# Kernel optimization log

Hardware: AMD Instinct MI355X
Metric: run time of the kernel (lower is better)

Reference implementation:

```python
import jax, jax.numpy as jnp
import numpy as np

B, L, D, H = 4, 1024, 1024, 16
DH = D // H  # 64
TOPK = 32


def setup_inputs() -> dict:
    key = jax.random.key(0)
    ks = jax.random.split(key, 9)
    s = 1.0 / np.sqrt(D)
    return {
        "x": jax.random.normal(ks[0], (B, L, D), jnp.float32),
        "Wq": jax.random.normal(ks[1], (D, D), jnp.float32) * s,
        "bq": jax.random.normal(ks[2], (D,), jnp.float32) * 0.01,
        "Wk": jax.random.normal(ks[3], (D, D), jnp.float32) * s,
        "bk": jax.random.normal(ks[4], (D,), jnp.float32) * 0.01,
        "Wv": jax.random.normal(ks[5], (D, D), jnp.float32) * s,
        "bv": jax.random.normal(ks[6], (D,), jnp.float32) * 0.01,
        "Wo": jax.random.normal(ks[7], (D, D), jnp.float32) * s,
        "bo": jax.random.normal(ks[8], (D,), jnp.float32) * 0.01,
        "top_k": TOPK,
    }


def reference(x, Wq, bq, Wk, bk, Wv, bv, Wo, bo, top_k):
    b, l, _ = x.shape
    q = (x @ Wq + bq).reshape(b, l, H, DH)
    k = (x @ Wk + bk).reshape(b, l, H, DH)
    v = (x @ Wv + bv).reshape(b, l, H, DH)
    # scores: [B, i, j, h]
    scores = jnp.einsum('bihd,bjhd->bijh', q, k) / np.sqrt(DH).astype(np.float32)
    # softmax over axis 2 (j), as in the original (dim=2 of bijh)
    weights = jax.nn.softmax(scores, axis=2)
    if top_k is not None:
        # top-k along j: move j to last axis -> [B, i, h, j]
        w_t = jnp.swapaxes(weights, 2, 3)
        _, idx = jax.lax.top_k(w_t, top_k)
        mask = jnp.put_along_axis(jnp.zeros_like(w_t), idx, 1.0, axis=-1, inplace=False)
        w_t = w_t * mask
        w_t = w_t / (jnp.sum(w_t, axis=-1, keepdims=True) + 1e-8)
        weights = jnp.swapaxes(w_t, 2, 3)
    attn = jnp.einsum('bijh,bjhd->bihd', weights, v).reshape(b, l, D)
    return attn @ Wo + bo
```

## Files before the change

### kernel.cpp

```cpp
#include <hip/hip_runtime.h>
#include <math.h>

#define B_ 4
#define L_ 1024
#define D_ 1024
#define H_ 16
#define DH_ 64
#define M_ (B_*L_)

typedef _Float16 half8 __attribute__((ext_vector_type(8)));
typedef _Float16 half4 __attribute__((ext_vector_type(4)));
typedef float f32x4 __attribute__((ext_vector_type(4)));

#define MFMA16(a,b,c) __builtin_amdgcn_mfma_f32_16x16x32_f16(a, b, c, 0, 0, 0)

__device__ __forceinline__ void glds16(const void* g, const void* s) {
  __builtin_amdgcn_global_load_lds(
      (const __attribute__((address_space(1))) uint32_t*)g,
      (__attribute__((address_space(3))) uint32_t*)(uintptr_t)s,
      16, 0, 0);
}

#define DPPF(oldv, x, ctrl, rmask) \
  __int_as_float(__builtin_amdgcn_update_dpp(__float_as_int(oldv), __float_as_int(x), ctrl, rmask, 0xf, false))

__device__ __forceinline__ float wfred_max(float x) {
  x = fmaxf(x, DPPF(-INFINITY, x, 0x111, 0xf));
  x = fmaxf(x, DPPF(-INFINITY, x, 0x112, 0xf));
  x = fmaxf(x, DPPF(-INFINITY, x, 0x114, 0xf));
  x = fmaxf(x, DPPF(-INFINITY, x, 0x118, 0xf));
  x = fmaxf(x, DPPF(-INFINITY, x, 0x142, 0xa));
  x = fmaxf(x, DPPF(-INFINITY, x, 0x143, 0xc));
  return __int_as_float(__builtin_amdgcn_readlane(__float_as_int(x), 63));
}
__device__ __forceinline__ float wfred_sum(float x) {
  x = x + DPPF(0.f, x, 0x111, 0xf);
  x = x + DPPF(0.f, x, 0x112, 0xf);
  x = x + DPPF(0.f, x, 0x114, 0xf);
  x = x + DPPF(0.f, x, 0x118, 0xf);
  x = x + DPPF(0.f, x, 0x142, 0xa);
  x = x + DPPF(0.f, x, 0x143, 0xc);
  return __int_as_float(__builtin_amdgcn_readlane(__float_as_int(x), 63));
}

__global__ __launch_bounds__(256) void split_x(const float* __restrict__ x,
                                               _Float16* __restrict__ xh,
                                               _Float16* __restrict__ xl) {
  const int i = blockIdx.x * 256 + threadIdx.x;
  float4 v = ((const float4*)x)[i];
  const float a0 = v.x * 16.f, a1 = v.y * 16.f, a2 = v.z * 16.f, a3 = v.w * 16.f;
  const _Float16 h0 = (_Float16)a0, h1 = (_Float16)a1, h2 = (_Float16)a2, h3 = (_Float16)a3;
  half4 hv, lv;
  hv[0] = h0; hv[1] = h1; hv[2] = h2; hv[3] = h3;
  lv[0] = (_Float16)(a0 - (float)h0);
  lv[1] = (_Float16)(a1 - (float)h1);
  lv[2] = (_Float16)(a2 - (float)h2);
  lv[3] = (_Float16)(a3 - (float)h3);
  ((half4*)xh)[i] = hv;
  ((half4*)xl)[i] = lv;
}

__global__ __launch_bounds__(256) void split_w4(const float* __restrict__ W0,
                                                const float* __restrict__ W1,
                                                const float* __restrict__ W2,
                                                const float* __restrict__ W3,
                                                _Float16* __restrict__ Whl_base) {
  const int z = blockIdx.z;
  const float* W = (z == 0) ? W0 : (z == 1) ? W1 : (z == 2) ? W2 : W3;
  _Float16* Wh = Whl_base + (size_t)z * 2 * (size_t)(D_ * D_);
  _Float16* Wl = Wh + (size_t)(D_ * D_);
  __shared__ float tile[64][65];
  const int t = threadIdx.x;
  const int tk = blockIdx.x & 15;
  const int tn = blockIdx.x >> 4;
  const int kr = t >> 2, ns = (t & 3) * 16;
  const float* src = W + (size_t)(tk * 64 + kr) * D_ + tn * 64 + ns;
  float4 v0 = ((const float4*)src)[0];
  float4 v1 = ((const float4*)src)[1];
  float4 v2 = ((const float4*)src)[2];
  float4 v3 = ((const float4*)src)[3];
  tile[ns + 0][kr] = v0.x;  tile[ns + 1][kr] = v0.y;  tile[ns + 2][kr] = v0.z;  tile[ns + 3][kr] = v0.w;
  tile[ns + 4][kr] = v1.x;  tile[ns + 5][kr] = v1.y;  tile[ns + 6][kr] = v1.z;  tile[ns + 7][kr] = v1.w;
  tile[ns + 8][kr] = v2.x;  tile[ns + 9][kr] = v2.y;  tile[ns + 10][kr] = v2.z; tile[ns + 11][kr] = v2.w;
  tile[ns + 12][kr] = v3.x; tile[ns + 13][kr] = v3.y; tile[ns + 14][kr] = v3.z; tile[ns + 15][kr] = v3.w;
  __syncthreads();
  const int nr = t >> 2, ks = (t & 3) * 16;
  const float* tr = &tile[nr][ks];
  half8 hv0, hv1, lv0, lv1;
#pragma unroll
  for (int i = 0; i < 8; i++) {
    const float s0 = tr[i] * 512.f;
    const float s1 = tr[i + 8] * 512.f;
    const _Float16 h0 = (_Float16)s0, h1 = (_Float16)s1;
    hv0[i] = h0; hv1[i] = h1;
    lv0[i] = (_Float16)(s0 - (float)h0);
    lv1[i] = (_Float16)(s1 - (float)h1);
  }
  _Float16* dh = Wh + (size_t)(tn * 64 + nr) * D_ + tk * 64 + ks;
  _Float16* dl = Wl + (size_t)(tn * 64 + nr) * D_ + tk * 64 + ks;
  *(half8*)dh = hv0; *(half8*)(dh + 8) = hv1;
  *(half8*)dl = lv0; *(half8*)(dl + 8) = lv1;
}

__device__ __forceinline__ void gemm_f16x3_body(
    const _Float16* __restrict__ Ah, const _Float16* __restrict__ Al,
    const _Float16* __restrict__ Bh, const _Float16* __restrict__ Bl,
    const float* __restrict__ bias, float* __restrict__ Cf,
    _Float16* __restrict__ Ch, _Float16* __restrict__ Cl, const bool f16out) {
  __shared__ __align__(16) _Float16 sA[2][2][128][32];
  __shared__ __align__(16) _Float16 sB[2][2][128][32];
  const int t = threadIdx.x;
  const int lane = t & 63;
  const int wid = t >> 6;
  const int bm = blockIdx.y * 128;
  const int bn = blockIdx.x * 128;

  const int m0 = t >> 2, sp0 = t & 3;
  const int sl0 = sp0 ^ ((m0 >> 1) & 3);
  const int m1 = m0 + 64;
  const _Float16* gA0h = Ah + (size_t)(bm + m0) * D_ + sl0 * 8;
  const _Float16* gA1h = Ah + (size_t)(bm + m1) * D_ + sl0 * 8;
  const _Float16* gA0l = Al + (size_t)(bm + m0) * D_ + sl0 * 8;
  const _Float16* gA1l = Al + (size_t)(bm + m1) * D_ + sl0 * 8;
  const _Float16* gB0h = Bh + (size_t)(bn + m0) * D_ + sl0 * 8;
  const _Float16* gB1h = Bh + (size_t)(bn + m1) * D_ + sl0 * 8;
  const _Float16* gB0l = Bl + (size_t)(bn + m0) * D_ + sl0 * 8;
  const _Float16* gB1l = Bl + (size_t)(bn + m1) * D_ + sl0 * 8;

  char* sAb = (char*)&sA[0][0][0][0];
  char* sBb = (char*)&sB[0][0][0][0];
  const int wvb = (t >> 6) * 1024;

#define STAGE(pp, kk) do { \
    glds16(gA0h + (kk), sAb + (pp) * 16384 + wvb); \
    glds16(gA1h + (kk), sAb + (pp) * 16384 + 4096 + wvb); \
    glds16(gA0l + (kk), sAb + (pp) * 16384 + 8192 + wvb); \
    glds16(gA1l + (kk), sAb + (pp) * 16384 + 12288 + wvb); \
    glds16(gB0h + (kk), sBb + (pp) * 16384 + wvb); \
    glds16(gB1h + (kk), sBb + (pp) * 16384 + 4096 + wvb); \
    glds16(gB0l + (kk), sBb + (pp) * 16384 + 8192 + wvb); \
    glds16(gB1l + (kk), sBb + (pp) * 16384 + 12288 + wvb); \
  } while (0)

  STAGE(0, 0);
  __syncthreads();

  f32x4 acc[4][4];
#pragma unroll
  for (int i = 0; i < 4; i++)
#pragma unroll
    for (int j = 0; j < 4; j++) acc[i][j] = {0.f, 0.f, 0.f, 0.f};

  const int wr = wid >> 1, wc = wid & 1;
  const int l15 = lane & 15;
  const int soff = ((lane >> 4) ^ ((l15 >> 1) & 3)) * 8;

  int p = 0;
  for (int k0 = 0; k0 < 1024; k0 += 32) {
    const bool more = (k0 + 32) < 1024;
    if (more) STAGE(p ^ 1, k0 + 32);
    half8 bh[4], bl[4];
#pragma unroll
    for (int ni = 0; ni < 4; ni++) {
      const int rb = wc * 64 + ni * 16 + l15;
      bh[ni] = *(const half8*)&sB[p][0][rb][soff];
      bl[ni] = *(const half8*)&sB[p][1][rb][soff];
    }
#pragma unroll
    for (int mi = 0; mi < 4; mi++) {
      const int ra = wr * 64 + mi * 16 + l15;
      const half8 ah = *(const half8*)&sA[p][0][ra][soff];
      const half8 al = *(const half8*)&sA[p][1][ra][soff];
#pragma unroll
      for (int ni = 0; ni < 4; ni++) {
        acc[mi][ni] = MFMA16(ah, bh[ni], acc[mi][ni]);
        acc[mi][ni] = MFMA16(ah, bl[ni], acc[mi][ni]);
        acc[mi][ni] = MFMA16(al, bh[ni], acc[mi][ni]);
      }
    }
    if (more) {
      __syncthreads();
      p ^= 1;
    }
  }
#undef STAGE

  const float inv = 1.0f / 8192.0f;
  const int orow = bm + wr * 64 + (lane >> 4) * 4;
  const int ocol = bn + wc * 64 + l15;
#pragma unroll
  for (int ni = 0; ni < 4; ni++) {
    const int col = ocol + ni * 16;
    const float bv = bias[col];
#pragma unroll
    for (int mi = 0; mi < 4; mi++) {
      const f32x4 a = acc[mi][ni];
#pragma unroll
      for (int r = 0; r < 4; r++) {
        const size_t idx = (size_t)(orow + mi * 16 + r) * D_ + col;
        const float val = a[r] * inv + bv;
        if (f16out) {
          const float vs = val * 16.0f;
          const _Float16 hh = (_Float16)vs;
          Ch[idx] = hh;
          Cl[idx] = (_Float16)(vs - (float)hh);
        } else {
          Cf[idx] = val;
        }
      }
    }
  }
}

__global__ __launch_bounds__(256, 2) void gemm_qkv_f16(
    const _Float16* __restrict__ xh, const _Float16* __restrict__ xl,
    const _Float16* __restrict__ Whq, const _Float16* __restrict__ Wlq,
    const _Float16* __restrict__ Whk, const _Float16* __restrict__ Wlk,
    const _Float16* __restrict__ Whv, const _Float16* __restrict__ Wlv,
    const float* __restrict__ bq, const float* __restrict__ bk, const float* __restrict__ bv,
    _Float16* __restrict__ qh, _Float16* __restrict__ ql,
    _Float16* __restrict__ kh, _Float16* __restrict__ kl,
    float* __restrict__ vf) {
  const int z = blockIdx.z;
  const _Float16* Bh = (z == 0) ? Whq : (z == 1) ? Whk : Whv;
  const _Float16* Bl = (z == 0) ? Wlq : (z == 1) ? Wlk : Wlv;
  const float* bias = (z == 0) ? bq : (z == 1) ? bk : bv;
  if (z == 2) {
    gemm_f16x3_body(xh, xl, Bh, Bl, bias, vf, nullptr, nullptr, false);
  } else {
    _Float16* Ch = (z == 0) ? qh : kh;
    _Float16* Cl = (z == 0) ? ql : kl;
    gemm_f16x3_body(xh, xl, Bh, Bl, bias, nullptr, Ch, Cl, true);
  }
}

__global__ __launch_bounds__(256, 2) void gemm_out_f16(
    const _Float16* __restrict__ ah, const _Float16* __restrict__ al,
    const _Float16* __restrict__ bh, const _Float16* __restrict__ bl,
    const float* __restrict__ bias, float* __restrict__ C) {
  gemm_f16x3_body(ah, al, bh, bl, bias, C, nullptr, nullptr, false);
}

#define SSWZ(row) (((row) & 7) << 2)

__global__ __launch_bounds__(512, 4) void attn_topk_mfma(
    const _Float16* __restrict__ qh, const _Float16* __restrict__ ql,
    const _Float16* __restrict__ kh, const _Float16* __restrict__ kl,
    const float* __restrict__ vf,
    _Float16* __restrict__ awh, _Float16* __restrict__ awl) {
  __shared__ float S[8][1024];
  __shared__ int   cidx[8][64];
  __shared__ float cfe[8][64];
  const int t = threadIdx.x;
  const int lane = t & 63;
  const int w = t >> 6;
  const int id = blockIdx.x;
  const int wk = (id & 7) * 1024 + (id >> 3);
  const int it = wk & 127;
  const int bh = wk >> 7;
  const int h = bh & 15;
  const int b = bh >> 4;
  const int i0 = it * 8;
  const size_t rowbase = (size_t)b * L_;
  const int l15 = lane & 15;
  const int kgrp = lane >> 4;

  half8 Ahf[2], Alf[2];
#pragma unroll
  for (int ks = 0; ks < 2; ks++) {
    const size_t off = (rowbase + i0 + (l15 & 7)) * D_ + h * DH_ + ks * 32 + kgrp * 8;
    Ahf[ks] = *(const half8*)(qh + off);
    Alf[ks] = *(const half8*)(ql + off);
  }

  const float sscale = 1.0f / 2048.0f;
  for (int jt = 0; jt < 8; jt++) {
    const int j0 = w * 128 + jt * 16;
    const size_t koff = (rowbase + j0 + l15) * D_ + h * DH_ + kgrp * 8;
    const half8 Bh0 = *(const half8*)(kh + koff);
    const half8 Bh1 = *(const half8*)(kh + koff + 32);
    const half8 Bl0 = *(const half8*)(kl + koff);
    const half8 Bl1 = *(const half8*)(kl + koff + 32);
    f32x4 acc = {0.f, 0.f, 0.f, 0.f};
    acc = MFMA16(Ahf[0], Bh0, acc);
    acc = MFMA16(Ahf[1], Bh1, acc);
    acc = MFMA16(Ahf[0], Bl0, acc);
    acc = MFMA16(Ahf[1], Bl1, acc);
    acc = MFMA16(Alf[0], Bh0, acc);
    acc = MFMA16(Alf[1], Bh1, acc);
    if (kgrp < 2) {
      const int srow = kgrp * 4;
#pragma unroll
      for (int r = 0; r < 4; r++)
        S[srow + r][(j0 + l15) ^ SSWZ(srow + r)] = acc[r] * sscale;
    }
  }
  __syncthreads();

  const int row = w;
  const int swz = SSWZ(row);
  float sc[16];
#pragma unroll
  for (int u = 0; u < 16; u++) sc[u] = S[row][(u * 64 + lane) ^ swz];

  float mx;
  {
    float m = sc[0];
#pragma unroll
    for (int u = 1; u < 16; u++) m = fmaxf(m, sc[u]);
    mx = wfred_max(m);
  }

  float lo = mx - 16.f, hi = mx;
  for (int it2 = 0; it2 < 12; ++it2) {
    float mid = 0.5f * (lo + hi);
    int cnt = 0;
#pragma unroll
    for (int u = 0; u < 16; u++) cnt += __popcll(__ballot(sc[u] >= mid));
    if (cnt >= 32) lo = mid; else hi = mid;
  }
  int cabove = 0;
#pragma unroll
  for (int u = 0; u < 16; u++) cabove += __popcll(__ballot(sc[u] >= hi));
  float v31 = hi;
  while (cabove < 32) {
    float nx = -INFINITY;
#pragma unroll
    for (int u = 0; u < 16; u++) nx = fmaxf(nx, (sc[u] < v31) ? sc[u] : -INFINITY);
    nx = wfred_max(nx);
    int ceq = 0;
#pragma unroll
    for (int u = 0; u < 16; u++) ceq += __popcll(__ballot(sc[u] == nx));
    cabove += ceq;
    v31 = nx;
  }
  int c_eq = 0;
#pragma unroll
  for (int u = 0; u < 16; u++) c_eq += __popcll(__ballot(sc[u] == v31));
  const int c_gt = cabove - c_eq;
  const bool span = (cabove > 32);
  const int keep_eq = 32 - c_gt;
  float v32;
  if (span) {
    v32 = v31;
  } else {
    float nx = -INFINITY;
#pragma unroll
    for (int u = 0; u < 16; u++) nx = fmaxf(nx, (sc[u] < v31) ? sc[u] : -INFINITY);
    nx = wfred_max(nx);
    v32 = nx;
  }
  const float tau = 0.5f * (v31 + v32);
  const float invbeta = 166666.67f;

  float e_[16];
#pragma unroll
  for (int u = 0; u < 16; u++) e_[u] = __expf(sc[u] - mx);
  float z = 0.f;
#pragma unroll
  for (int u = 0; u < 16; u++) z += e_[u];
  z = wfred_sum(z);

  bool band = false;
  if (!span) {
    int inband = 0;
#pragma unroll
    for (int u = 0; u < 16; u++)
      inband |= (fabsf(sc[u] - tau) <= 1.81e-4f) ? 1 : 0;
    band = (__ballot(inband) != 0ull);
  }

  const float cutoff = fminf(tau - 1.8e-4f, v31);
  const float* vcol = vf + rowbase * D_ + h * DH_ + lane;
  float o;
  bool fast = false;
  if (!span) {
    int run = 0;
    float psum = 0.f;
#pragma unroll
    for (int u = 0; u < 16; u++) {
      unsigned long long m = __ballot(sc[u] >= cutoff);
      if (sc[u] >= cutoff) {
        float feu;
        if (band) {
          float arg = (sc[u] - tau) * invbeta;
          float fwv = (arg > 30.f) ? 1.f : ((arg < -30.f) ? 0.f : 1.f / (1.f + __expf(-arg)));
          feu = fwv * e_[u];
        } else {
          feu = (sc[u] > tau) ? e_[u] : 0.f;
        }
        int pos = run + (int)__popcll(m & ((1ull << lane) - 1ull));
        if (pos < 64) { cidx[row][pos] = u * 64 + lane; cfe[row][pos] = feu; }
        psum += feu;
      }
      run += (int)__popcll(m);
    }
    if (run <= 64) {
      fast = true;
      const int npad = (run + 7) & ~7;
      if (lane < npad - run) { cidx[row][run + lane] = 0; cfe[row][run + lane] = 0.f; }
      const int nch = npad >> 3;
      auto ldc = [&](int c, int* J, float* F) {
#pragma unroll
        for (int i = 0; i < 8; i++) { J[i] = cidx[row][c * 8 + i]; F[i] = cfe[row][c * 8 + i]; }
      };
      auto ldv = [&](const int* J, float* V) {
#pragma unroll
        for (int i = 0; i < 8; i++) V[i] = vcol[(size_t)J[i] * D_];
      };
      auto fm8 = [&](const float* F, const float* V, float& a) {
#pragma unroll
        for (int i = 0; i < 8; i++) a = fmaf(F[i], V[i], a);
      };
      int jA[8], jB[8]; float fA[8], fB[8], vA[8], vB[8];
      float accv = 0.f;
      ldc(0, jA, fA); ldv(jA, vA);
      for (int c = 0; c < nch; c += 2) {
        if (c + 1 < nch) { ldc(c + 1, jB, fB); ldv(jB, vB); }
        fm8(fA, vA, accv);
        if (c + 2 < nch) { ldc(c + 2, jA, fA); ldv(jA, vA); }
        if (c + 1 < nch) fm8(fB, vB, accv);
      }
      const float Ssum = wfred_sum(psum);
      o = accv / (Ssum + 1e-8f * z);
    }
  }
  if (!fast) {
    float Ssum = 0.f, acc = 0.f;
    int eq_seen = 0;
    for (int u = 0; u < 16; ++u) {
      unsigned long long mask = __ballot(sc[u] >= cutoff);
      while (mask) {
        int l2 = (int)__builtin_ctzll(mask);
        mask &= mask - 1;
        float s_ = __shfl(sc[u], l2, 64);
        float e2 = __expf(s_ - mx);
        float f_;
        if (span) {
          if (s_ > v31) f_ = 1.f;
          else if (s_ == v31) { f_ = (eq_seen < keep_eq) ? 1.f : 0.f; ++eq_seen; }
          else f_ = 0.f;
        } else {
          float arg = (s_ - tau) * invbeta;
          f_ = (arg > 30.f) ? 1.f : ((arg < -30.f) ? 0.f : 1.f / (1.f + __expf(-arg)));
        }
        float fe_ = f_ * e2;
        Ssum += fe_;
        acc = fmaf(fe_, vcol[(size_t)(u * 64 + l2) * D_], acc);
      }
    }
    o = acc / (Ssum + 1e-8f * z);
  }

  const float os = o * 16.0f;
  const _Float16 oh = (_Float16)os;
  const size_t oidx = (rowbase + i0 + row) * D_ + h * DH_ + lane;
  awh[oidx] = oh;
  awl[oidx] = (_Float16)(os - (float)oh);
}

extern "C" void kernel_launch(void* const* d_in, const int* in_sizes, int n_in,
                              void* d_out, int out_size, void* d_ws, size_t ws_size,
                              hipStream_t stream) {
  const float* x  = (const float*)d_in[0];
  const float* Wq = (const float*)d_in[1];
  const float* bq = (const float*)d_in[2];
  const float* Wk = (const float*)d_in[3];
  const float* bk = (const float*)d_in[4];
  const float* Wv = (const float*)d_in[5];
  const float* bv = (const float*)d_in[6];
  const float* Wo = (const float*)d_in[7];
  const float* bo = (const float*)d_in[8];
  float* out = (float*)d_out;

  const size_t MD = (size_t)M_ * D_;
  const size_t WD = (size_t)D_ * D_;
  float* slot0 = (float*)d_ws;
  float* slot1 = slot0 + MD;
  float* vf    = slot1 + MD;
  float* slot3 = vf + MD;
  float* slot4 = slot3 + MD;

  _Float16* qh = (_Float16*)slot0;  _Float16* ql = qh + MD;
  _Float16* kh = (_Float16*)slot1;  _Float16* kl = kh + MD;
  _Float16* xh = (_Float16*)slot3;  _Float16* xl = xh + MD;
  _Float16* awh = xh;
  _Float16* awl = xl;
  _Float16* Wsplit = (_Float16*)slot4;
  _Float16* Whq = Wsplit;
  _Float16* Wlq = Whq + WD;
  _Float16* Whk = Wlq + WD;
  _Float16* Wlk = Whk + WD;
  _Float16* Whv = Wlk + WD;
  _Float16* Wlv = Whv + WD;
  _Float16* Who = Wlv + WD;
  _Float16* Wlo = Who + WD;

  dim3 b256(256);
  hipLaunchKernelGGL(split_x, dim3(4096), b256, 0, stream, x, xh, xl);
  hipLaunchKernelGGL(split_w4, dim3(256, 1, 4), b256, 0, stream, Wq, Wk, Wv, Wo, Wsplit);
  hipLaunchKernelGGL(gemm_qkv_f16, dim3(8, 32, 3), b256, 0, stream,
                     xh, xl, Whq, Wlq, Whk, Wlk, Whv, Wlv, bq, bk, bv,
                     qh, ql, kh, kl, vf);
  hipLaunchKernelGGL(attn_topk_mfma, dim3(8192), dim3(512), 0, stream,
                     qh, ql, kh, kl, vf, awh, awl);
  hipLaunchKernelGGL(gemm_out_f16, dim3(8, 32), b256, 0, stream,
                     awh, awl, Who, Wlo, bo, out);
}
```

Baseline: 504.9 us.

## Single-buffer GEMM LDS for higher occupancy, pack attention candidates, add MFMA priority

Result: slower. 529.6 us (+4.9%).

```diff
diff --git a/kernel.cpp b/kernel.cpp
--- a/kernel.cpp
+++ b/kernel.cpp
@@ -107,8 +107,8 @@
     const _Float16* __restrict__ Bh, const _Float16* __restrict__ Bl,
     const float* __restrict__ bias, float* __restrict__ Cf,
     _Float16* __restrict__ Ch, _Float16* __restrict__ Cl, const bool f16out) {
-  __shared__ __align__(16) _Float16 sA[2][2][128][32];
-  __shared__ __align__(16) _Float16 sB[2][2][128][32];
+  __shared__ __align__(16) _Float16 sA[2][128][32];
+  __shared__ __align__(16) _Float16 sB[2][128][32];
   const int t = threadIdx.x;
   const int lane = t & 63;
   const int wid = t >> 6;
@@ -127,23 +127,20 @@
   const _Float16* gB0l = Bl + (size_t)(bn + m0) * D_ + sl0 * 8;
   const _Float16* gB1l = Bl + (size_t)(bn + m1) * D_ + sl0 * 8;
 
-  char* sAb = (char*)&sA[0][0][0][0];
-  char* sBb = (char*)&sB[0][0][0][0];
-  const int wvb = (t >> 6) * 1024;
-
-#define STAGE(pp, kk) do { \
-    glds16(gA0h + (kk), sAb + (pp) * 16384 + wvb); \
-    glds16(gA1h + (kk), sAb + (pp) * 16384 + 4096 + wvb); \
-    glds16(gA0l + (kk), sAb + (pp) * 16384 + 8192 + wvb); \
-    glds16(gA1l + (kk), sAb + (pp) * 16384 + 12288 + wvb); \
-    glds16(gB0h + (kk), sBb + (pp) * 16384 + wvb); \
-    glds16(gB1h + (kk), sBb + (pp) * 16384 + 4096 + wvb); \
-    glds16(gB0l + (kk), sBb + (pp) * 16384 + 8192 + wvb); \
-    glds16(gB1l + (kk), sBb + (pp) * 16384 + 12288 + wvb); \
+  char* sAb = (char*)&sA[0][0][0];
+  char* sBb = (char*)&sB[0][0][0];
+  const int wvb = wid * 1024;
+
+#define STAGE(kk) do { \
+    glds16(gA0h + (kk), sAb + wvb); \
+    glds16(gA1h + (kk), sAb + 4096 + wvb); \
+    glds16(gA0l + (kk), sAb + 8192 + wvb); \
+    glds16(gA1l + (kk), sAb + 12288 + wvb); \
+    glds16(gB0h + (kk), sBb + wvb); \
+    glds16(gB1h + (kk), sBb + 4096 + wvb); \
+    glds16(gB0l + (kk), sBb + 8192 + wvb); \
+    glds16(gB1l + (kk), sBb + 12288 + wvb); \
   } while (0)
-
-  STAGE(0, 0);
-  __syncthreads();
 
   f32x4 acc[4][4];
 #pragma unroll
@@ -155,32 +152,28 @@
   const int l15 = lane & 15;
   const int soff = ((lane >> 4) ^ ((l15 >> 1) & 3)) * 8;
 
-  int p = 0;
   for (int k0 = 0; k0 < 1024; k0 += 32) {
-    const bool more = (k0 + 32) < 1024;
-    if (more) STAGE(p ^ 1, k0 + 32);
+    if (k0) __syncthreads();
+    STAGE(k0);
+    __syncthreads();
     half8 bh[4], bl[4];
 #pragma unroll
     for (int ni = 0; ni < 4; ni++) {
       const int rb = wc * 64 + ni * 16 + l15;
-      bh[ni] = *(const half8*)&sB[p][0][rb][soff];
-      bl[ni] = *(const half8*)&sB[p][1][rb][soff];
+      bh[ni] = *(const half8*)&sB[0][rb][soff];
+      bl[ni] = *(const half8*)&sB[1][rb][soff];
     }
 #pragma unroll
     for (int mi = 0; mi < 4; mi++) {
       const int ra = wr * 64 + mi * 16 + l15;
-      const half8 ah = *(const half8*)&sA[p][0][ra][soff];
-      const half8 al = *(const half8*)&sA[p][1][ra][soff];
+      const half8 ah = *(const half8*)&sA[0][ra][soff];
+      const half8 al = *(const half8*)&sA[1][ra][soff];
 #pragma unroll
       for (int ni = 0; ni < 4; ni++) {
         acc[mi][ni] = MFMA16(ah, bh[ni], acc[mi][ni]);
         acc[mi][ni] = MFMA16(ah, bl[ni], acc[mi][ni]);
         acc[mi][ni] = MFMA16(al, bh[ni], acc[mi][ni]);
       }
-    }
-    if (more) {
-      __syncthreads();
-      p ^= 1;
     }
   }
 #undef STAGE
@@ -212,7 +205,7 @@
   }
 }
 
-__global__ __launch_bounds__(256, 2) void gemm_qkv_f16(
+__global__ __launch_bounds__(256, 4) void gemm_qkv_f16(
     const _Float16* __restrict__ xh, const _Float16* __restrict__ xl,
     const _Float16* __restrict__ Whq, const _Float16* __restrict__ Wlq,
     const _Float16* __restrict__ Whk, const _Float16* __restrict__ Wlk,
@@ -234,7 +227,7 @@
   }
 }
 
-__global__ __launch_bounds__(256, 2) void gemm_out_f16(
+__global__ __launch_bounds__(256, 4) void gemm_out_f16(
     const _Float16* __restrict__ ah, const _Float16* __restrict__ al,
     const _Float16* __restrict__ bh, const _Float16* __restrict__ bl,
     const float* __restrict__ bias, float* __restrict__ C) {
@@ -249,8 +242,7 @@
     const float* __restrict__ vf,
     _Float16* __restrict__ awh, _Float16* __restrict__ awl) {
   __shared__ float S[8][1024];
-  __shared__ int   cidx[8][64];
-  __shared__ float cfe[8][64];
+  __shared__ float cp[8][64][2];
   const int t = threadIdx.x;
   const int lane = t & 63;
   const int w = t >> 6;
@@ -282,12 +274,14 @@
     const half8 Bl0 = *(const half8*)(kl + koff);
     const half8 Bl1 = *(const half8*)(kl + koff + 32);
     f32x4 acc = {0.f, 0.f, 0.f, 0.f};
+    __builtin_amdgcn_s_setprio(1);
     acc = MFMA16(Ahf[0], Bh0, acc);
     acc = MFMA16(Ahf[1], Bh1, acc);
     acc = MFMA16(Ahf[0], Bl0, acc);
     acc = MFMA16(Ahf[1], Bl1, acc);
     acc = MFMA16(Alf[0], Bh0, acc);
     acc = MFMA16(Alf[1], Bh1, acc);
+    __builtin_amdgcn_s_setprio(0);
     if (kgrp < 2) {
       const int srow = kgrp * 4;
 #pragma unroll
@@ -390,7 +384,10 @@
           feu = (sc[u] > tau) ? e_[u] : 0.f;
         }
         int pos = run + (int)__popcll(m & ((1ull << lane) - 1ull));
-        if (pos < 64) { cidx[row][pos] = u * 64 + lane; cfe[row][pos] = feu; }
+        if (pos < 64) {
+          float2 pk; pk.x = __int_as_float(u * 64 + lane); pk.y = feu;
+          *(float2*)&cp[row][pos][0] = pk;
+        }
         psum += feu;
       }
       run += (int)__popcll(m);
@@ -398,11 +395,17 @@
     if (run <= 64) {
       fast = true;
       const int npad = (run + 7) & ~7;
-      if (lane < npad - run) { cidx[row][run + lane] = 0; cfe[row][run + lane] = 0.f; }
+      if (lane < npad - run) {
+        float2 pk; pk.x = __int_as_float(0); pk.y = 0.f;
+        *(float2*)&cp[row][run + lane][0] = pk;
+      }
       const int nch = npad >> 3;
       auto ldc = [&](int c, int* J, float* F) {
 #pragma unroll
-        for (int i = 0; i < 8; i++) { J[i] = cidx[row][c * 8 + i]; F[i] = cfe[row][c * 8 + i]; }
+        for (int i = 0; i < 8; i++) {
+          float2 pk = *(float2*)&cp[row][c * 8 + i][0];
+          J[i] = __float_as_int(pk.x); F[i] = pk.y;
+        }
       };
       auto ldv = [&](const int* J, float* V) {
 #pragma unroll
```
